# Kernel tuning notes

Measured on AMD Instinct MI355X. Metric: run time of the kernel, lower is better.

Reference implementation:

```python
import jax, jax.numpy as jnp
import numpy as np

N_NODES = 50000
GAMMA = -0.5
ZETA = 1.1
DEBUG_VAR = 1e-07


def setup_inputs() -> dict:
    key = jax.random.key(0)
    ks = jax.random.split(key, 8)
    N, E, D, H = N_NODES, 800000, 256, 128
    s = 0.05
    return {
        "x": jax.random.normal(ks[0], (N, D), jnp.float32),
        "W_nb": jax.random.normal(ks[1], (D, H), jnp.float32) * s,
        "b_nb": jnp.zeros((H,), jnp.float32),
        "W_self": jax.random.normal(ks[2], (D, H), jnp.float32) * s,
        "b_self": jnp.zeros((H,), jnp.float32),
        "W_att": jax.random.normal(ks[3], (2 * H, 1), jnp.float32) * s,
        "b_att": jnp.zeros((1,), jnp.float32),
        "values": jax.random.uniform(ks[4], (E,), jnp.float32),
        "noise": jax.random.uniform(ks[5], (E, 1), jnp.float32),
        "row": jax.random.randint(ks[6], (E,), 0, N, jnp.int32),
        "col": jax.random.randint(ks[7], (E,), 0, N, jnp.int32),
    }


def reference(x, W_nb, b_nb, W_self, b_self, W_att, b_att, values, noise, row, col):
    # edge gather + tiny attention MLP
    f1 = jax.nn.relu(x[row] @ W_nb + b_nb)      # [E, H]
    f2 = jax.nn.relu(x[col] @ W_self + b_self)  # [E, H]
    log_alpha = jnp.concatenate([f1, f2], axis=1) @ W_att + b_att  # [E, 1]

    # hard-concrete sample (training=True), beta=1.0
    u = noise + DEBUG_VAR
    gate = jax.nn.sigmoid(jnp.log(u) - jnp.log(1.0 - u) + log_alpha)
    mask = jnp.clip(gate * (ZETA - GAMMA) + GAMMA, 0.0, 1.0)[:, 0]  # [E]

    masked_values = values * mask

    # degree-normalized scatter: rowsum then symmetric D^{-1/2} A D^{-1/2}
    rowsum = jax.ops.segment_sum(masked_values, row, num_segments=N_NODES) + 1e-10
    d_inv_sqrt = jnp.power(rowsum, -0.5)
    d_inv_sqrt = jnp.where(jnp.isinf(d_inv_sqrt), 0.0, d_inv_sqrt)

    norm_values = masked_values * d_inv_sqrt[row] * d_inv_sqrt[col]  # [E]
    return norm_values
```

## Files before the change

kernel.cpp:

```cpp
#include <hip/hip_runtime.h>
#include <hip/hip_bf16.h>

typedef __attribute__((ext_vector_type(8))) short bf16x8;
typedef __attribute__((ext_vector_type(4))) float f32x4;

#define D_DIM 256
#define H_DIM 128
#define QSH 12544
#define NSL 128

__device__ inline ushort f2bf(float f) {
    union { float f; unsigned u; } a; a.f = f;
    unsigned r = a.u + 0x7fffu + ((a.u >> 16) & 1u);
    return (ushort)(r >> 16);
}
__device__ inline float bf2f(unsigned hi16) {
    union { unsigned u; float f; } a; a.u = hi16 << 16;
    return a.f;
}

__global__ void k0_init(const float* __restrict__ W_nb, const float* __restrict__ W_self,
                        ushort* __restrict__ Wt, float* __restrict__ dis, int N, int init_dis) {
    int i = blockIdx.x * 256 + threadIdx.x;
    if (i < 2 * H_DIM * D_DIM) {
        int j    = i & 7;
        int lane = (i >> 3) & 63;
        int ks   = (i >> 9) & 7;
        int ni   = (i >> 12) & 3;
        int cg   = i >> 14;
        int li   = lane & 15;
        int grp  = lane >> 4;
        int h    = (cg & 1) * 64 + ni * 16 + li;
        int k    = ks * 32 + grp * 8 + j;
        const float* W = (cg >> 1) ? W_self : W_nb;
        Wt[i] = f2bf(W[k * H_DIM + h]);
    }
    if (init_dis && i < N) dis[i] = 1e-10f;
}

__global__ __launch_bounds__(512, 2) void k1_gemm(
    const float* __restrict__ x, const ushort* __restrict__ Wt,
    const float* __restrict__ b_nb, const float* __restrict__ b_self,
    const float* __restrict__ W_att,
    float* __restrict__ g_nb, float* __restrict__ g_self, int N, int ntiles)
{
    __shared__ __align__(16) ushort A_lds[64][264];
    __shared__ float part[2][2][64];

    const int t    = threadIdx.x;
    const int lane = t & 63;
    const int w    = t >> 6;
    const int rh   = w >> 2;
    const int cg   = w & 3;
    const int br   = cg >> 1;
    const int ch   = cg & 1;
    const int li   = lane & 15;
    const int grp  = lane >> 4;

    float bias[4], aw[4];
    #pragma unroll
    for (int ni = 0; ni < 4; ni++) {
        int hh = ch * 64 + ni * 16 + li;
        bias[ni] = br ? b_self[hh] : b_nb[hh];
        aw[ni]   = W_att[br * H_DIM + hh];
    }

    bf16x8 Bf[4][8];
    #pragma unroll
    for (int ni = 0; ni < 4; ni++)
        #pragma unroll
        for (int ks = 0; ks < 8; ks++)
            Bf[ni][ks] = *reinterpret_cast<const bf16x8*>(
                Wt + (((size_t)(cg * 4 + ni) * 8 + ks) << 9) + lane * 8);

    const int sr = t >> 3;
    const int sc = t & 7;

    for (int rt = blockIdx.x; rt < ntiles; rt += gridDim.x) {
        const int row0 = rt * 64;

        __syncthreads();
        {
            const int gr = row0 + sr;
            const bool v = gr < N;
            const float4* src = reinterpret_cast<const float4*>(x + (size_t)gr * D_DIM);
            #pragma unroll
            for (int j = 0; j < 8; j++) {
                int c4 = sc + j * 8;
                ushort4 o;
                if (v) {
                    float4 f = src[c4];
                    o.x = f2bf(f.x); o.y = f2bf(f.y); o.z = f2bf(f.z); o.w = f2bf(f.w);
                } else { o.x = 0; o.y = 0; o.z = 0; o.w = 0; }
                *reinterpret_cast<ushort4*>(&A_lds[sr][c4 * 4]) = o;
            }
        }
        __syncthreads();

        f32x4 acc[2][4];
        #pragma unroll
        for (int mi = 0; mi < 2; mi++)
            #pragma unroll
            for (int ni = 0; ni < 4; ni++) acc[mi][ni] = f32x4{0.f, 0.f, 0.f, 0.f};

        #pragma unroll
        for (int ks = 0; ks < 8; ks++) {
            bf16x8 af0 = *reinterpret_cast<const bf16x8*>(&A_lds[rh * 32 + li][ks * 32 + grp * 8]);
            bf16x8 af1 = *reinterpret_cast<const bf16x8*>(&A_lds[rh * 32 + 16 + li][ks * 32 + grp * 8]);
            #pragma unroll
            for (int ni = 0; ni < 4; ni++) {
                acc[0][ni] = __builtin_amdgcn_mfma_f32_16x16x32_bf16(af0, Bf[ni][ks], acc[0][ni], 0, 0, 0);
                acc[1][ni] = __builtin_amdgcn_mfma_f32_16x16x32_bf16(af1, Bf[ni][ks], acc[1][ni], 0, 0, 0);
            }
        }

        float p[2][4];
        #pragma unroll
        for (int mi = 0; mi < 2; mi++)
            #pragma unroll
            for (int r4 = 0; r4 < 4; r4++) p[mi][r4] = 0.f;
        #pragma unroll
        for (int ni = 0; ni < 4; ni++)
            #pragma unroll
            for (int mi = 0; mi < 2; mi++)
                #pragma unroll
                for (int r4 = 0; r4 < 4; r4++) {
                    float y = acc[mi][ni][r4] + bias[ni];
                    y = y > 0.f ? y : 0.f;
                    p[mi][r4] += y * aw[ni];
                }
        #pragma unroll
        for (int mi = 0; mi < 2; mi++)
            #pragma unroll
            for (int r4 = 0; r4 < 4; r4++) {
                float v = p[mi][r4];
                #pragma unroll
                for (int m = 1; m < 16; m <<= 1) v += __shfl_xor(v, m);
                if (li == 0)
                    part[br][ch][rh * 32 + mi * 16 + grp * 4 + r4] = v;
            }
        __syncthreads();

        if (t < 128) {
            int b_ = t >> 6, lr = t & 63;
            int gr = row0 + lr;
            if (gr < N) {
                float val = part[b_][0][lr] + part[b_][1][lr];
                if (b_) g_self[gr] = val; else g_nb[gr] = val;
            }
        }
    }
}

__global__ __launch_bounds__(256) void k2a_gate(
    const int* __restrict__ row, const int* __restrict__ col,
    const float* __restrict__ values, const float* __restrict__ noise,
    const float* __restrict__ g_nb, const float* __restrict__ g_self,
    const float* __restrict__ b_att, float* __restrict__ mv_out, int E)
{
    int i = (blockIdx.x * 256 + threadIdx.x) * 4;
    if (i >= E) return;
    const float ba = b_att[0];
    if (i + 3 < E) {
        int4   r4 = *reinterpret_cast<const int4*>(row + i);
        int4   c4 = *reinterpret_cast<const int4*>(col + i);
        float4 v4 = *reinterpret_cast<const float4*>(values + i);
        float4 u4 = *reinterpret_cast<const float4*>(noise + i);
        int   rr[4] = { r4.x, r4.y, r4.z, r4.w };
        int   cc[4] = { c4.x, c4.y, c4.z, c4.w };
        float vv[4] = { v4.x, v4.y, v4.z, v4.w };
        float uu[4] = { u4.x, u4.y, u4.z, u4.w };
        float gn[4], gs[4];
        #pragma unroll
        for (int j = 0; j < 4; j++) { gn[j] = g_nb[rr[j]]; gs[j] = g_self[cc[j]]; }
        float m[4];
        #pragma unroll
        for (int j = 0; j < 4; j++) {
            float u    = uu[j] + 1e-7f;
            float la   = gn[j] + gs[j] + ba;
            float gate = u / (u + (1.f - u) * __expf(-la));
            float mask = fminf(fmaxf(gate * 1.6f - 0.5f, 0.f), 1.f);
            m[j] = vv[j] * mask;
        }
        *reinterpret_cast<float4*>(mv_out + i) = make_float4(m[0], m[1], m[2], m[3]);
    } else {
        for (int j = 0; j < 4 && i + j < E; j++) {
            int e = i + j;
            float u    = noise[e] + 1e-7f;
            float la   = g_nb[row[e]] + g_self[col[e]] + ba;
            float gate = u / (u + (1.f - u) * __expf(-la));
            float mask = fminf(fmaxf(gate * 1.6f - 0.5f, 0.f), 1.f);
            mv_out[e] = values[e] * mask;
        }
    }
}

__global__ __launch_bounds__(1024) void k2q_scatter(
    const int* __restrict__ row, const float* __restrict__ mv,
    ushort* __restrict__ priv, int E, int ES)
{
    __shared__ float acc[QSH];
    const int s  = blockIdx.x >> 2;
    const int q  = blockIdx.x & 3;
    const int t  = threadIdx.x;
    const int lo = q * QSH;

    for (int i = t; i < QSH; i += 1024) acc[i] = 0.f;
    __syncthreads();

    const int base = s * ES;
    int end = base + ES; if (end > E) end = E;

    int i = base + t * 4;
    for (; i + 3 < end; i += 4096) {
        int4   r4 = *reinterpret_cast<const int4*>(row + i);
        float4 m4 = *reinterpret_cast<const float4*>(mv + i);
        int d;
        d = r4.x - lo; if ((unsigned)d < (unsigned)QSH && m4.x != 0.f) atomicAdd(&acc[d], m4.x);
        d = r4.y - lo; if ((unsigned)d < (unsigned)QSH && m4.y != 0.f) atomicAdd(&acc[d], m4.y);
        d = r4.z - lo; if ((unsigned)d < (unsigned)QSH && m4.z != 0.f) atomicAdd(&acc[d], m4.z);
        d = r4.w - lo; if ((unsigned)d < (unsigned)QSH && m4.w != 0.f) atomicAdd(&acc[d], m4.w);
    }
    for (; i < end; i++) {
        int d = row[i] - lo;
        float m = mv[i];
        if ((unsigned)d < (unsigned)QSH && m != 0.f) atomicAdd(&acc[d], m);
    }
    __syncthreads();

    ushort* dst = priv + (size_t)s * (4 * QSH) + lo;
    for (int j = t * 2; j < QSH; j += 2048) {
        unsigned pk = (unsigned)f2bf(acc[j]) | ((unsigned)f2bf(acc[j + 1]) << 16);
        *reinterpret_cast<unsigned*>(dst + j) = pk;
    }
}

__global__ __launch_bounds__(256) void k2c_reduce(
    const ushort* __restrict__ priv, float* __restrict__ dis, int N)
{
    int n0 = (blockIdx.x * 256 + threadIdx.x) * 2;
    if (n0 >= N) return;
    float s0 = 1e-10f, s1 = 1e-10f;
    for (int p = 0; p < NSL; p++) {
        unsigned v = *reinterpret_cast<const unsigned*>(priv + (size_t)p * (4 * QSH) + n0);
        s0 += bf2f(v & 0xffffu);
        s1 += bf2f(v >> 16);
    }
    dis[n0] = rsqrtf(s0);
    if (n0 + 1 < N) dis[n0 + 1] = rsqrtf(s1);
}

__global__ __launch_bounds__(256) void k2_atomic_fb(
    const int* __restrict__ row, const int* __restrict__ col,
    const float* __restrict__ values, const float* __restrict__ noise,
    const float* __restrict__ g_nb, const float* __restrict__ g_self,
    const float* __restrict__ b_att,
    float* __restrict__ out, float* __restrict__ dis, int E)
{
    int e = blockIdx.x * 256 + threadIdx.x;
    if (e >= E) return;
    int   r = row[e], c = col[e];
    float u = noise[e] + 1e-7f;
    float la = g_nb[r] + g_self[c] + b_att[0];
    float gate = u / (u + (1.f - u) * __expf(-la));
    float mask = fminf(fmaxf(gate * 1.6f - 0.5f, 0.f), 1.f);
    float m = values[e] * mask;
    out[e] = m;
    if (m != 0.f) atomicAdd(&dis[r], m);
}
__global__ __launch_bounds__(256) void k2c_rsqrt_fb(float* __restrict__ dis, int N)
{
    int n = blockIdx.x * 256 + threadIdx.x;
    if (n < N) dis[n] = rsqrtf(dis[n]);
}

__global__ __launch_bounds__(256) void k3_edge2(
    const int* __restrict__ row, const int* __restrict__ col,
    float* __restrict__ out, const float* __restrict__ dis, int E)
{
    int i = (blockIdx.x * 256 + threadIdx.x) * 4;
    if (i >= E) return;
    if (i + 3 < E) {
        int4   r4 = *reinterpret_cast<const int4*>(row + i);
        int4   c4 = *reinterpret_cast<const int4*>(col + i);
        float4 m4 = *reinterpret_cast<const float4*>(out + i);
        float dr0 = dis[r4.x], dc0 = dis[c4.x];
        float dr1 = dis[r4.y], dc1 = dis[c4.y];
        float dr2 = dis[r4.z], dc2 = dis[c4.z];
        float dr3 = dis[r4.w], dc3 = dis[c4.w];
        float4 o;
        o.x = m4.x * dr0 * dc0;
        o.y = m4.y * dr1 * dc1;
        o.z = m4.z * dr2 * dc2;
        o.w = m4.w * dr3 * dc3;
        *reinterpret_cast<float4*>(out + i) = o;
    } else {
        for (int j = 0; j < 4 && i + j < E; j++) {
            int e = i + j;
            out[e] = out[e] * dis[row[e]] * dis[col[e]];
        }
    }
}

extern "C" void kernel_launch(void* const* d_in, const int* in_sizes, int n_in,
                              void* d_out, int out_size, void* d_ws, size_t ws_size,
                              hipStream_t stream) {
    const float* x      = (const float*)d_in[0];
    const float* W_nb   = (const float*)d_in[1];
    const float* b_nb   = (const float*)d_in[2];
    const float* W_self = (const float*)d_in[3];
    const float* b_self = (const float*)d_in[4];
    const float* W_att  = (const float*)d_in[5];
    const float* b_att  = (const float*)d_in[6];
    const float* values = (const float*)d_in[7];
    const float* noise  = (const float*)d_in[8];
    const int*   row    = (const int*)d_in[9];
    const int*   col    = (const int*)d_in[10];

    const int N = in_sizes[0] / D_DIM;
    const int E = in_sizes[7];
    float* out = (float*)d_out;

    char* ws = (char*)d_ws;
    ushort* Wt     = (ushort*)ws;
    float*  g_nb   = (float*)(ws + 131072);
    float*  g_self = g_nb + N;
    float*  dis    = g_self + N;
    ushort* priv   = (ushort*)(dis + N);

    int ES = ((E + NSL - 1) / NSL + 3) & ~3;
    size_t need = 131072 + (size_t)3 * N * 4 + (size_t)NSL * 4 * QSH * 2;
    bool lds_path = (N <= 4 * QSH) && (need <= ws_size);

    int init_n = 2 * H_DIM * D_DIM;
    if (N > init_n) init_n = N;
    k0_init<<<(init_n + 255) / 256, 256, 0, stream>>>(W_nb, W_self, Wt, dis, N, lds_path ? 0 : 1);

    const int ntiles = (N + 63) / 64;
    k1_gemm<<<256, 512, 0, stream>>>(x, Wt, b_nb, b_self, W_att, g_nb, g_self, N, ntiles);

    int eb4 = ((E + 3) / 4 + 255) / 256;
    if (lds_path) {
        k2a_gate<<<eb4, 256, 0, stream>>>(row, col, values, noise, g_nb, g_self, b_att, out, E);
        k2q_scatter<<<NSL * 4, 1024, 0, stream>>>(row, out, priv, E, ES);
        k2c_reduce<<<((N + 1) / 2 + 255) / 256, 256, 0, stream>>>(priv, dis, N);
    } else {
        k2_atomic_fb<<<(E + 255) / 256, 256, 0, stream>>>(row, col, values, noise,
                                                          g_nb, g_self, b_att, out, dis, E);
        k2c_rsqrt_fb<<<(N + 255) / 256, 256, 0, stream>>>(dis, N);
    }

    k3_edge2<<<eb4, 256, 0, stream>>>(row, col, out, dis, E);
}
```

Before: 66.93 us.

## Pack row+bf16 mask for scatter and stage bf16 degree table in LDS

The gate kernel now also writes a packed 32-bit word holding the row index in the high 16 bits and the bf16 masked value in the low 16 bits. The scatter kernel reads one array instead of two, which halves its input traffic across the 512 blocks that each rescan the edge slice. The degree inverse-sqrt is stored as bf16, and the final edge kernel loads the whole table into LDS per block so the random row/col lookups hit shared memory instead of global memory. This costs precision (bf16 degree values and masked values in the sum) and an extra E-sized buffer, and packing the row into 16 bits relies on N being at most 4*QSH, which the lds_path check already enforces.

```diff
diff --git a/kernel.cpp b/kernel.cpp
--- a/kernel.cpp
+++ b/kernel.cpp
@@ -8,6 +8,7 @@
 #define H_DIM 128
 #define QSH 12544
 #define NSL 128
+#define NMAXL (4 * QSH)
 
 __device__ inline ushort f2bf(float f) {
     union { float f; unsigned u; } a; a.f = f;
@@ -156,7 +157,8 @@
     const int* __restrict__ row, const int* __restrict__ col,
     const float* __restrict__ values, const float* __restrict__ noise,
     const float* __restrict__ g_nb, const float* __restrict__ g_self,
-    const float* __restrict__ b_att, float* __restrict__ mv_out, int E)
+    const float* __restrict__ b_att, float* __restrict__ mv_out,
+    unsigned* __restrict__ pk, int E)
 {
     int i = (blockIdx.x * 256 + threadIdx.x) * 4;
     if (i >= E) return;
@@ -173,7 +175,7 @@
         float gn[4], gs[4];
         #pragma unroll
         for (int j = 0; j < 4; j++) { gn[j] = g_nb[rr[j]]; gs[j] = g_self[cc[j]]; }
-        float m[4];
+        float m[4]; unsigned pkv[4];
         #pragma unroll
         for (int j = 0; j < 4; j++) {
             float u    = uu[j] + 1e-7f;
@@ -181,23 +183,27 @@
             float gate = u / (u + (1.f - u) * __expf(-la));
             float mask = fminf(fmaxf(gate * 1.6f - 0.5f, 0.f), 1.f);
             m[j] = vv[j] * mask;
+            pkv[j] = ((unsigned)rr[j] << 16) | (unsigned)f2bf(m[j]);
         }
         *reinterpret_cast<float4*>(mv_out + i) = make_float4(m[0], m[1], m[2], m[3]);
+        *reinterpret_cast<uint4*>(pk + i) = make_uint4(pkv[0], pkv[1], pkv[2], pkv[3]);
     } else {
         for (int j = 0; j < 4 && i + j < E; j++) {
             int e = i + j;
+            int   r = row[e];
             float u    = noise[e] + 1e-7f;
-            float la   = g_nb[row[e]] + g_self[col[e]] + ba;
+            float la   = g_nb[r] + g_self[col[e]] + ba;
             float gate = u / (u + (1.f - u) * __expf(-la));
             float mask = fminf(fmaxf(gate * 1.6f - 0.5f, 0.f), 1.f);
-            mv_out[e] = values[e] * mask;
+            float m = values[e] * mask;
+            mv_out[e] = m;
+            pk[e] = ((unsigned)r << 16) | (unsigned)f2bf(m);
         }
     }
 }
 
 __global__ __launch_bounds__(1024) void k2q_scatter(
-    const int* __restrict__ row, const float* __restrict__ mv,
-    ushort* __restrict__ priv, int E, int ES)
+    const unsigned* __restrict__ pk, ushort* __restrict__ priv, int E, int ES)
 {
     __shared__ float acc[QSH];
     const int s  = blockIdx.x >> 2;
@@ -213,30 +219,34 @@
 
     int i = base + t * 4;
     for (; i + 3 < end; i += 4096) {
-        int4   r4 = *reinterpret_cast<const int4*>(row + i);
-        float4 m4 = *reinterpret_cast<const float4*>(mv + i);
-        int d;
-        d = r4.x - lo; if ((unsigned)d < (unsigned)QSH && m4.x != 0.f) atomicAdd(&acc[d], m4.x);
-        d = r4.y - lo; if ((unsigned)d < (unsigned)QSH && m4.y != 0.f) atomicAdd(&acc[d], m4.y);
-        d = r4.z - lo; if ((unsigned)d < (unsigned)QSH && m4.z != 0.f) atomicAdd(&acc[d], m4.z);
-        d = r4.w - lo; if ((unsigned)d < (unsigned)QSH && m4.w != 0.f) atomicAdd(&acc[d], m4.w);
+        uint4 p4 = *reinterpret_cast<const uint4*>(pk + i);
+        unsigned p; int d; float m;
+        p = p4.x; d = (int)(p >> 16) - lo; m = bf2f(p & 0xffffu);
+        if ((unsigned)d < (unsigned)QSH && m != 0.f) atomicAdd(&acc[d], m);
+        p = p4.y; d = (int)(p >> 16) - lo; m = bf2f(p & 0xffffu);
+        if ((unsigned)d < (unsigned)QSH && m != 0.f) atomicAdd(&acc[d], m);
+        p = p4.z; d = (int)(p >> 16) - lo; m = bf2f(p & 0xffffu);
+        if ((unsigned)d < (unsigned)QSH && m != 0.f) atomicAdd(&acc[d], m);
+        p = p4.w; d = (int)(p >> 16) - lo; m = bf2f(p & 0xffffu);
+        if ((unsigned)d < (unsigned)QSH && m != 0.f) atomicAdd(&acc[d], m);
     }
     for (; i < end; i++) {
-        int d = row[i] - lo;
-        float m = mv[i];
+        unsigned p = pk[i];
+        int d = (int)(p >> 16) - lo;
+        float m = bf2f(p & 0xffffu);
         if ((unsigned)d < (unsigned)QSH && m != 0.f) atomicAdd(&acc[d], m);
     }
     __syncthreads();
 
     ushort* dst = priv + (size_t)s * (4 * QSH) + lo;
     for (int j = t * 2; j < QSH; j += 2048) {
-        unsigned pk = (unsigned)f2bf(acc[j]) | ((unsigned)f2bf(acc[j + 1]) << 16);
-        *reinterpret_cast<unsigned*>(dst + j) = pk;
+        unsigned pkk = (unsigned)f2bf(acc[j]) | ((unsigned)f2bf(acc[j + 1]) << 16);
+        *reinterpret_cast<unsigned*>(dst + j) = pkk;
     }
 }
 
 __global__ __launch_bounds__(256) void k2c_reduce(
-    const ushort* __restrict__ priv, float* __restrict__ dis, int N)
+    const ushort* __restrict__ priv, ushort* __restrict__ disb, int N)
 {
     int n0 = (blockIdx.x * 256 + threadIdx.x) * 2;
     if (n0 >= N) return;
@@ -246,8 +256,42 @@
         s0 += bf2f(v & 0xffffu);
         s1 += bf2f(v >> 16);
     }
-    dis[n0] = rsqrtf(s0);
-    if (n0 + 1 < N) dis[n0 + 1] = rsqrtf(s1);
+    unsigned o = (unsigned)f2bf(rsqrtf(s0)) | ((unsigned)f2bf(rsqrtf(s1)) << 16);
+    *reinterpret_cast<unsigned*>(disb + n0) = o;
+}
+
+__global__ __launch_bounds__(1024) void k3_edge2_lds(
+    const int* __restrict__ row, const int* __restrict__ col,
+    float* __restrict__ out, const ushort* __restrict__ disb,
+    int Npad2, int E, int EB)
+{
+    __shared__ ushort ldis[NMAXL];
+    const int t = threadIdx.x;
+    {
+        const unsigned* src = reinterpret_cast<const unsigned*>(disb);
+        unsigned* dst = reinterpret_cast<unsigned*>(ldis);
+        const int nw = Npad2 >> 1;
+        for (int i = t; i < nw; i += 1024) dst[i] = src[i];
+    }
+    __syncthreads();
+
+    const int base = blockIdx.x * EB;
+    int end = base + EB; if (end > E) end = E;
+
+    int i = base + t * 4;
+    for (; i + 3 < end; i += 4096) {
+        int4   r4 = *reinterpret_cast<const int4*>(row + i);
+        int4   c4 = *reinterpret_cast<const int4*>(col + i);
+        float4 m4 = *reinterpret_cast<const float4*>(out + i);
+        float4 o;
+        o.x = m4.x * bf2f(ldis[r4.x]) * bf2f(ldis[c4.x]);
+        o.y = m4.y * bf2f(ldis[r4.y]) * bf2f(ldis[c4.y]);
+        o.z = m4.z * bf2f(ldis[r4.z]) * bf2f(ldis[c4.z]);
+        o.w = m4.w * bf2f(ldis[r4.w]) * bf2f(ldis[c4.w]);
+        *reinterpret_cast<float4*>(out + i) = o;
+    }
+    for (; i < end; i++)
+        out[i] = out[i] * bf2f(ldis[row[i]]) * bf2f(ldis[col[i]]);
 }
 
 __global__ __launch_bounds__(256) void k2_atomic_fb(
@@ -273,33 +317,13 @@
     int n = blockIdx.x * 256 + threadIdx.x;
     if (n < N) dis[n] = rsqrtf(dis[n]);
 }
-
-__global__ __launch_bounds__(256) void k3_edge2(
+__global__ __launch_bounds__(256) void k3_edge2_fb(
     const int* __restrict__ row, const int* __restrict__ col,
     float* __restrict__ out, const float* __restrict__ dis, int E)
 {
-    int i = (blockIdx.x * 256 + threadIdx.x) * 4;
-    if (i >= E) return;
-    if (i + 3 < E) {
-        int4   r4 = *reinterpret_cast<const int4*>(row + i);
-        int4   c4 = *reinterpret_cast<const int4*>(col + i);
-        float4 m4 = *reinterpret_cast<const float4*>(out + i);
-        float dr0 = dis[r4.x], dc0 = dis[c4.x];
-        float dr1 = dis[r4.y], dc1 = dis[c4.y];
-        float dr2 = dis[r4.z], dc2 = dis[c4.z];
-        float dr3 = dis[r4.w], dc3 = dis[c4.w];
-        float4 o;
-        o.x = m4.x * dr0 * dc0;
-        o.y = m4.y * dr1 * dc1;
-        o.z = m4.z * dr2 * dc2;
-        o.w = m4.w * dr3 * dc3;
-        *reinterpret_cast<float4*>(out + i) = o;
-    } else {
-        for (int j = 0; j < 4 && i + j < E; j++) {
-            int e = i + j;
-            out[e] = out[e] * dis[row[e]] * dis[col[e]];
-        }
-    }
+    int e = blockIdx.x * 256 + threadIdx.x;
+    if (e >= E) return;
+    out[e] = out[e] * dis[row[e]] * dis[col[e]];
 }
 
 extern "C" void kernel_launch(void* const* d_in, const int* in_sizes, int n_in,
@@ -326,11 +350,16 @@
     float*  g_nb   = (float*)(ws + 131072);
     float*  g_self = g_nb + N;
     float*  dis    = g_self + N;
+    ushort* disb   = (ushort*)dis;
     ushort* priv   = (ushort*)(dis + N);
-
+    size_t pk_off  = 131072 + (size_t)3 * N * 4 + (size_t)NSL * NMAXL * 2;
+    pk_off = (pk_off + 15) & ~(size_t)15;
+    unsigned* pk   = (unsigned*)(ws + pk_off);
+
+    const int Npad2 = (N + 1) & ~1;
     int ES = ((E + NSL - 1) / NSL + 3) & ~3;
-    size_t need = 131072 + (size_t)3 * N * 4 + (size_t)NSL * 4 * QSH * 2;
-    bool lds_path = (N <= 4 * QSH) && (need <= ws_size);
+    size_t need = pk_off + (size_t)E * 4;
+    bool lds_path = (N <= NMAXL) && (need <= ws_size);
 
     int init_n = 2 * H_DIM * D_DIM;
     if (N > init_n) init_n = N;
@@ -339,16 +368,18 @@
     const int ntiles = (N + 63) / 64;
     k1_gemm<<<256, 512, 0, stream>>>(x, Wt, b_nb, b_self, W_att, g_nb, g_self, N, ntiles);
 
-    int eb4 = ((E + 3) / 4 + 255) / 256;
     if (lds_path) {
-        k2a_gate<<<eb4, 256, 0, stream>>>(row, col, values, noise, g_nb, g_self, b_att, out, E);
-        k2q_scatter<<<NSL * 4, 1024, 0, stream>>>(row, out, priv, E, ES);
-        k2c_reduce<<<((N + 1) / 2 + 255) / 256, 256, 0, stream>>>(priv, dis, N);
+        int eb4 = ((E + 3) / 4 + 255) / 256;
+        k2a_gate<<<eb4, 256, 0, stream>>>(row, col, values, noise, g_nb, g_self,
+                                          b_att, out, pk, E);
+        k2q_scatter<<<NSL * 4, 1024, 0, stream>>>(pk, priv, E, ES);
+        k2c_reduce<<<((N + 1) / 2 + 255) / 256, 256, 0, stream>>>(priv, disb, N);
+        int EB = ((E + 255) / 256 + 3) & ~3;
+        k3_edge2_lds<<<256, 1024, 0, stream>>>(row, col, out, disb, Npad2, E, EB);
     } else {
         k2_atomic_fb<<<(E + 255) / 256, 256, 0, stream>>>(row, col, values, noise,
                                                           g_nb, g_self, b_att, out, dis, E);
         k2c_rsqrt_fb<<<(N + 255) / 256, 256, 0, stream>>>(dis, N);
-    }
-
-    k3_edge2<<<eb4, 256, 0, stream>>>(row, col, out, dis, E);
-}
+        k3_edge2_fb<<<(E + 255) / 256, 256, 0, stream>>>(row, col, out, dis, E);
+    }
+}
```

After: 62.37 us. 6.8% less time.
